# Optimization experiments

Hardware: AMD Instinct MI355X
Metric: run time of the kernel (lower is better)

## Reference

```python
import jax, jax.numpy as jnp
import numpy as np

N, E = 50000, 800000
D_IN, H, D_OUT = 100, 128, 40
N_MID = 2  # num_layers(5) - 3
EPS = 1e-5


def setup_inputs() -> dict:
    key = jax.random.key(0)
    ks = iter(jax.random.split(key, 40))
    rn = lambda shape, s=0.05: jax.random.normal(next(ks), shape, dtype=jnp.float32) * s
    inp = {
        "x": jax.random.normal(next(ks), (N, D_IN), dtype=jnp.float32),
        "edge_index": jax.random.randint(next(ks), (2, E), 0, N, dtype=jnp.int64),
        "percent": 70,
        "ricci_curvature": jax.random.normal(next(ks), (E,), dtype=jnp.float32),
        # GCNConv weights/biases
        "W1": rn((D_IN, H)), "b1": jnp.zeros((H,), jnp.float32),
        "W2": rn((D_IN + H, H)), "b2": jnp.zeros((H,), jnp.float32),
        "Wm": rn((N_MID, 2 * H, H)), "bm": jnp.zeros((N_MID, H), jnp.float32),
        "Wo": rn((2 * H, D_OUT)), "bo": jnp.zeros((D_OUT,), jnp.float32),
    }
    # BatchNorm1d params + running stats (eval mode)
    def bn_params(dim, lead=()):
        return (jnp.ones(lead + (dim,), jnp.float32),            # gamma
                jnp.zeros(lead + (dim,), jnp.float32),           # beta
                rn(lead + (dim,), 0.1),                          # running mean
                1.0 + 0.1 * jax.random.uniform(next(ks), lead + (dim,), dtype=jnp.float32))  # running var
    inp["bn1_g"], inp["bn1_b"], inp["bn1_m"], inp["bn1_v"] = bn_params(D_IN)
    inp["bn2_g"], inp["bn2_b"], inp["bn2_m"], inp["bn2_v"] = bn_params(D_IN + H)
    inp["bnm_g"], inp["bnm_b"], inp["bnm_m"], inp["bnm_v"] = bn_params(2 * H, (N_MID,))
    inp["bno_g"], inp["bno_b"], inp["bno_m"], inp["bno_v"] = bn_params(2 * H)
    return inp


def reference(x, edge_index, percent, ricci_curvature,
              W1, b1, W2, b2, Wm, bm, Wo, bo,
              bn1_g, bn1_b, bn1_m, bn1_v,
              bn2_g, bn2_b, bn2_m, bn2_v,
              bnm_g, bnm_b, bnm_m, bnm_v,
              bno_g, bno_b, bno_m, bno_v):
    # Eval mode: no sampling / dynamic edge weights, dropout = identity,
    # BN uses running stats. GCNConv = PyG: add self-loops, sym-norm D^-1/2 A D^-1/2.
    n = x.shape[0]
    loop = jnp.arange(n)
    src = jnp.concatenate([edge_index[0], loop])  # [E+N]
    dst = jnp.concatenate([edge_index[1], loop])
    deg = jnp.zeros((n,), x.dtype).at[dst].add(1.0)  # >=1 thanks to self-loops
    dis = jax.lax.rsqrt(deg)
    norm = (dis[src] * dis[dst])[:, None]  # [E+N, 1]

    def gcn(h, W, b):
        hw = h @ W  # [N, out]
        agg = jnp.zeros((n, W.shape[1]), h.dtype).at[dst].add(hw[src] * norm)
        return agg + b

    def bn(h, g, bta, m, v):
        return (h - m) * (g * jax.lax.rsqrt(v + EPS)) + bta

    res = []
    x_in = x
    h = jax.nn.relu(gcn(bn(x, bn1_g, bn1_b, bn1_m, bn1_v), W1, b1))
    res.append(h)
    h = jnp.concatenate([h, x_in], axis=1)  # [N, H+D_IN]
    h = jax.nn.relu(gcn(bn(h, bn2_g, bn2_b, bn2_m, bn2_v), W2, b2))
    res.append(h)
    h = jnp.concatenate([h, res[-2]], axis=1)  # [N, 2H]
    for i in range(Wm.shape[0]):
        hi = jax.nn.relu(gcn(bn(h, bnm_g[i], bnm_b[i], bnm_m[i], bnm_v[i]), Wm[i], bm[i]))
        res.append(hi)
        h = jnp.concatenate([hi, res[-2]], axis=1)
    out = gcn(bn(h, bno_g, bno_b, bno_m, bno_v), Wo, bo)
    return (out, *res)
```

## Files before the change

kernel.cpp:

```cpp
#include <hip/hip_runtime.h>
#include <hip/hip_bf16.h>
#include <cstdint>
#include <cstddef>

#define BN_EPS 1e-5f
typedef long long ll;
using bf16x8 = __attribute__((ext_vector_type(8))) short;
using f32x4  = __attribute__((ext_vector_type(4))) float;

__device__ __forceinline__ unsigned short f2bf(float f) {
    union { float f; unsigned u; } c; c.f = f;
    unsigned u = c.u;
    u += 0x7fff + ((u >> 16) & 1);
    return (unsigned short)(u >> 16);
}
__device__ __forceinline__ float bf2f(unsigned h) {
    union { unsigned u; float f; } c; c.u = h << 16;
    return c.f;
}
__device__ __forceinline__ void addbf8(float* a, uint4 v) {
    a[0] += bf2f(v.x & 0xffffu); a[1] += bf2f(v.x >> 16);
    a[2] += bf2f(v.y & 0xffffu); a[3] += bf2f(v.y >> 16);
    a[4] += bf2f(v.z & 0xffffu); a[5] += bf2f(v.z >> 16);
    a[6] += bf2f(v.w & 0xffffu); a[7] += bf2f(v.w >> 16);
}
__device__ __forceinline__ float4 bf4_to_f4(uint2 v) {
    return make_float4(bf2f(v.x & 0xffffu), bf2f(v.x >> 16),
                       bf2f(v.y & 0xffffu), bf2f(v.y >> 16));
}
__device__ __forceinline__ void gload_lds16(const void* g, void* lds) {
    __builtin_amdgcn_global_load_lds(
        (const __attribute__((address_space(1))) unsigned int*)g,
        (__attribute__((address_space(3))) unsigned int*)lds, 16, 0, 0);
}

__global__ void build0_kernel(const int* ei32, int* flag, int* deg, int* cursor, int N) {
    int i = blockIdx.x * 256 + threadIdx.x;
    if (i < N) { deg[i] = 1; cursor[i] = 0; }
    if (blockIdx.x == 0) {
        __shared__ int any;
        if (threadIdx.x == 0) any = 0;
        __syncthreads();
        for (int t = threadIdx.x; t < 2048; t += 256)
            if (ei32[2 * t + 1] != 0) any = 1;
        __syncthreads();
        if (threadIdx.x == 0) *flag = (any == 0) ? 1 : 0;
    }
}

__global__ void count_kernel(const void* ei, int E, int* deg, const int* flag) {
    int e = blockIdx.x * 256 + threadIdx.x;
    if (e >= E) return;
    int d = (*flag) ? (int)((const ll*)ei)[(size_t)E + e]
                    : ((const int*)ei)[(size_t)E + e];
    atomicAdd(&deg[d], 1);
}

__global__ __launch_bounds__(1024) void scanA_kernel(const int* deg, int* row_ptr,
                                                     int* bsum, float* dis, int N) {
    __shared__ int wsum[16];
    int i = blockIdx.x * 1024 + threadIdx.x;
    int lane = threadIdx.x & 63, wid = threadIdx.x >> 6;
    int dv = (i < N) ? deg[i] : 1;
    if (i < N) dis[i] = rsqrtf((float)dv);
    int v = (i < N) ? (dv - 1) : 0;
    int s = v;
#pragma unroll
    for (int o = 1; o < 64; o <<= 1) { int t = __shfl_up(s, o); if (lane >= o) s += t; }
    if (lane == 63) wsum[wid] = s;
    __syncthreads();
    if (threadIdx.x < 16) {
        int w = wsum[threadIdx.x];
        int ws_ = w;
#pragma unroll
        for (int o = 1; o < 16; o <<= 1) { int t = __shfl_up(ws_, o); if ((int)threadIdx.x >= o) ws_ += t; }
        wsum[threadIdx.x] = ws_ - w;
    }
    __syncthreads();
    s += wsum[wid];
    if (i < N) row_ptr[i + 1] = s;
    if (threadIdx.x == 1023) bsum[blockIdx.x] = s;
}

__global__ void scanB_kernel(int* bsum, int nb) {
    int lane = threadIdx.x;
    int v = (lane < nb) ? bsum[lane] : 0;
    int s = v;
#pragma unroll
    for (int o = 1; o < 64; o <<= 1) { int t = __shfl_up(s, o); if (lane >= o) s += t; }
    if (lane < nb) bsum[lane] = s - v;
}

__global__ __launch_bounds__(1024) void scanC_kernel(int* row_ptr, const int* bsum, int N) {
    int i = blockIdx.x * 1024 + threadIdx.x;
    if (i < N) row_ptr[i + 1] += bsum[blockIdx.x];
    if (i == 0) row_ptr[0] = 0;
}

__global__ void fill_kernel(const void* ei, int E, const int* row_ptr,
                            int* cursor, int* csr, const int* flag) {
    int e = blockIdx.x * 256 + threadIdx.x;
    if (e >= E) return;
    int s, d;
    if (*flag) { const ll* p = (const ll*)ei; s = (int)p[e]; d = (int)p[(size_t)E + e]; }
    else       { const int* p = (const int*)ei; s = p[e]; d = p[(size_t)E + e]; }
    int pos = atomicAdd(&cursor[d], 1);
    csr[row_ptr[d] + pos] = s;
}

struct LayerP {
    const float *W, *g, *b, *m, *v;
    int K, Dout, ncb, boff;
};
struct LayerPs { LayerP l[5]; };

__global__ __launch_bounds__(256) void fold_all(LayerPs P,
                                                unsigned short* __restrict__ Bhi,
                                                unsigned short* __restrict__ Blo,
                                                float* __restrict__ cvecA) {
    const LayerP& L = P.l[blockIdx.y];
    if (blockIdx.x < 128) {
        int nkc = (L.K + 63) >> 6 << 1;
        int total = nkc * L.ncb * 512;
        int idx = blockIdx.x * 256 + threadIdx.x;
        if (idx >= total) return;
        int i = idx & 7;
        int lane = (idx >> 3) & 63;
        int cb = (idx >> 9) % L.ncb;
        int kc = (idx >> 9) / L.ncb;
        int k = kc * 32 + (lane >> 4) * 8 + i;
        int col = cb * 16 + (lane & 15);
        float val = 0.f;
        if (k < L.K && col < L.Dout) {
            float s = L.g[k] * rsqrtf(L.v[k] + BN_EPS);
            val = L.W[k * L.Dout + col] * s;
        }
        unsigned short h = f2bf(val);
        Bhi[L.boff + idx] = h;
        Blo[L.boff + idx] = f2bf(val - bf2f(h));
    } else {
        int wid = threadIdx.x >> 6, lane = threadIdx.x & 63;
        int col = (blockIdx.x - 128) * 4 + wid;
        float acc = 0.f;
        if (col < L.Dout) {
            for (int k = lane; k < L.K; k += 64) {
                float s = L.g[k] * rsqrtf(L.v[k] + BN_EPS);
                acc += (L.b[k] - L.m[k] * s) * L.W[k * L.Dout + col];
            }
        }
#pragma unroll
        for (int o = 32; o >= 1; o >>= 1) acc += __shfl_xor(acc, o);
        if (lane == 0 && col < 128) cvecA[128 * blockIdx.y + col] = (col < L.Dout) ? acc : 0.f;
    }
}

__global__ __launch_bounds__(256, 4) void gemm_bf2_kernel(
    const unsigned short* __restrict__ X1, int K1, int ld1,
    const unsigned short* __restrict__ X2, int ld2,
    const unsigned short* __restrict__ Bhi, const unsigned short* __restrict__ Blo,
    const float* __restrict__ cvec, const float* __restrict__ dis,
    unsigned short* __restrict__ outp, int K, int N)
{
    __shared__ unsigned short Xs[2][64 * 64];
    const int tid = threadIdx.x;
    const int w = tid >> 6, lane = tid & 63;
    const int lr = lane & 15, lg = lane >> 4;
    const int brow = blockIdx.x * 64;
    const int nkt = (K + 63) >> 6;
    const int cb0 = 2 * w;

    int s_r[2], s_sl[2];
#pragma unroll
    for (int p = 0; p < 2; ++p) {
        int idx = p * 256 + tid;
        s_r[p] = idx >> 3;
        s_sl[p] = idx & 7;
    }

    auto STAGE = [&](int kt, int b) {
        const int k0 = kt * 64;
        const unsigned short* T = (k0 < K1) ? X1 : X2;
        const int ldT = (k0 < K1) ? ld1 : ld2;
        const int kb = (k0 < K1) ? k0 : (k0 - K1);
#pragma unroll
        for (int p = 0; p < 2; ++p) {
            int grow = brow + s_r[p]; if (grow >= N) grow = N - 1;
            int ksl = s_sl[p] ^ (s_r[p] & 7);
            gload_lds16(T + (size_t)grow * ldT + kb + ksl * 8,
                        (char*)Xs[b] + (size_t)(p * 256 + w * 64) * 16);
        }
    };

    f32x4 acc[4][2];
#pragma unroll
    for (int c = 0; c < 2; ++c) {
        float cv = cvec[(cb0 + c) * 16 + lr];
        f32x4 iv = {cv, cv, cv, cv};
#pragma unroll
        for (int rb = 0; rb < 4; ++rb) acc[rb][c] = iv;
    }

    STAGE(0, 0);
    for (int kt = 0; kt < nkt; ++kt) {
        const int cur = kt & 1;
        if (kt + 1 < nkt) STAGE(kt + 1, cur ^ 1);
        __builtin_amdgcn_sched_barrier(0);
        if (kt + 1 < nkt) asm volatile("s_waitcnt vmcnt(2)" ::: "memory");
        else              asm volatile("s_waitcnt vmcnt(0)" ::: "memory");
        __builtin_amdgcn_s_barrier();
        __builtin_amdgcn_sched_barrier(0);

#pragma unroll
        for (int ks = 0; ks < 2; ++ks) {
            const int kcg = kt * 2 + ks;
            bf16x8 a[4];
#pragma unroll
            for (int rb = 0; rb < 4; ++rb) {
                int r = rb * 16 + lr;
                a[rb] = *(const bf16x8*)((const char*)Xs[cur] + r * 128 +
                                         ((ks * 64 + lg * 16) ^ ((r & 7) << 4)));
            }
            const bf16x8* bh = (const bf16x8*)Bhi + (size_t)kcg * 8 * 64;
            const bf16x8* bl = (const bf16x8*)Blo + (size_t)kcg * 8 * 64;
#pragma unroll
            for (int c = 0; c < 2; ++c) {
                bf16x8 bhf = bh[(cb0 + c) * 64 + lane];
                bf16x8 blf = bl[(cb0 + c) * 64 + lane];
#pragma unroll
                for (int rb = 0; rb < 4; ++rb) {
                    acc[rb][c] = __builtin_amdgcn_mfma_f32_16x16x32_bf16(a[rb], bhf, acc[rb][c], 0, 0, 0);
                    acc[rb][c] = __builtin_amdgcn_mfma_f32_16x16x32_bf16(a[rb], blf, acc[rb][c], 0, 0, 0);
                }
            }
        }
        asm volatile("s_waitcnt lgkmcnt(0)" ::: "memory");
        __builtin_amdgcn_s_barrier();
        __builtin_amdgcn_sched_barrier(0);
    }

#pragma unroll
    for (int rb = 0; rb < 4; ++rb) {
#pragma unroll
        for (int r = 0; r < 4; ++r) {
            int grow = brow + rb * 16 + lg * 4 + r;
            if (grow >= N) continue;
            float d = dis[grow];
#pragma unroll
            for (int c = 0; c < 2; ++c)
                outp[(size_t)grow * 128 + (cb0 + c) * 16 + lr] = f2bf(d * acc[rb][c][r]);
        }
    }
}

template <bool B1, bool B2>
__global__ __launch_bounds__(256, 3) void gemm_mix2_kernel(
    const void* __restrict__ X1, int K1, int ld1,
    const void* __restrict__ X2, int ld2,
    const unsigned short* __restrict__ Bhi, const unsigned short* __restrict__ Blo,
    const float* __restrict__ cvec, const float* __restrict__ dis,
    unsigned short* __restrict__ outp, int K, int kc_lo, int N)
{
    __shared__ unsigned short Xhi[64 * 64];
    __shared__ unsigned short Xlo[64 * 64];
    const int tid = threadIdx.x;
    const int w = tid >> 6, lane = tid & 63;
    const int lr = lane & 15, lg = lane >> 4;
    const int brow = blockIdx.x * 64;
    const int nkt = (K + 63) >> 6;
    const int cb0 = 2 * w;

    f32x4 acc[4][2];
#pragma unroll
    for (int c = 0; c < 2; ++c) {
        float cv = cvec[(cb0 + c) * 16 + lr];
        f32x4 iv = {cv, cv, cv, cv};
#pragma unroll
        for (int rb = 0; rb < 4; ++rb) acc[rb][c] = iv;
    }

    for (int kt = 0; kt < nkt; ++kt) {
        const int k0 = kt * 64;
        const bool kt_lo = (kt * 2 + 1) >= kc_lo;
#pragma unroll
        for (int p = 0; p < 4; ++p) {
            int fidx = (p * 256 + tid) * 4;
            int r = fidx >> 6;
            int c = fidx & 63;
            int grow = brow + r;
            int k = k0 + c;
            float4 val = make_float4(0.f, 0.f, 0.f, 0.f);
            if (grow < N) {
                if (k < K1) {
                    if (B1) val = bf4_to_f4(*(const uint2*)((const unsigned short*)X1 + (size_t)grow * ld1 + k));
                    else    val = *(const float4*)((const float*)X1 + (size_t)grow * ld1 + k);
                } else if (k < K) {
                    int kk = k - K1;
                    if (B2) val = bf4_to_f4(*(const uint2*)((const unsigned short*)X2 + (size_t)grow * ld2 + kk));
                    else    val = *(const float4*)((const float*)X2 + (size_t)grow * ld2 + kk);
                }
            }
            unsigned short h0 = f2bf(val.x), h1 = f2bf(val.y),
                           h2 = f2bf(val.z), h3 = f2bf(val.w);
            int b8 = c * 2;
            int addr = r * 128 + (((b8 & 0x70) ^ ((r & 7) << 4)) | (b8 & 8));
            *(uint2*)((char*)Xhi + addr) =
                make_uint2((unsigned)h0 | ((unsigned)h1 << 16),
                           (unsigned)h2 | ((unsigned)h3 << 16));
            if (kt_lo) {
                unsigned short l0 = f2bf(val.x - bf2f(h0)), l1 = f2bf(val.y - bf2f(h1)),
                               l2 = f2bf(val.z - bf2f(h2)), l3 = f2bf(val.w - bf2f(h3));
                *(uint2*)((char*)Xlo + addr) =
                    make_uint2((unsigned)l0 | ((unsigned)l1 << 16),
                               (unsigned)l2 | ((unsigned)l3 << 16));
            }
        }
        __syncthreads();

#pragma unroll
        for (int ks = 0; ks < 2; ++ks) {
            const int kcg = kt * 2 + ks;
            const bool need_lo = (kcg >= kc_lo);
            bf16x8 ah[4], al[4];
#pragma unroll
            for (int rb = 0; rb < 4; ++rb) {
                int r = rb * 16 + lr;
                int off = ((ks * 64 + lg * 16) ^ ((r & 7) << 4));
                ah[rb] = *(const bf16x8*)((const char*)Xhi + r * 128 + off);
                if (need_lo) al[rb] = *(const bf16x8*)((const char*)Xlo + r * 128 + off);
            }
            const bf16x8* bh = (const bf16x8*)Bhi + (size_t)kcg * 8 * 64;
            const bf16x8* bl = (const bf16x8*)Blo + (size_t)kcg * 8 * 64;
#pragma unroll
            for (int c = 0; c < 2; ++c) {
                bf16x8 bhf = bh[(cb0 + c) * 64 + lane];
                bf16x8 blf = bl[(cb0 + c) * 64 + lane];
#pragma unroll
                for (int rb = 0; rb < 4; ++rb) {
                    acc[rb][c] = __builtin_amdgcn_mfma_f32_16x16x32_bf16(ah[rb], bhf, acc[rb][c], 0, 0, 0);
                    acc[rb][c] = __builtin_amdgcn_mfma_f32_16x16x32_bf16(ah[rb], blf, acc[rb][c], 0, 0, 0);
                    if (need_lo)
                        acc[rb][c] = __builtin_amdgcn_mfma_f32_16x16x32_bf16(al[rb], bhf, acc[rb][c], 0, 0, 0);
                }
            }
        }
        __syncthreads();
    }

#pragma unroll
    for (int rb = 0; rb < 4; ++rb) {
#pragma unroll
        for (int r = 0; r < 4; ++r) {
            int grow = brow + rb * 16 + lg * 4 + r;
            if (grow >= N) continue;
            float d = dis[grow];
#pragma unroll
            for (int c = 0; c < 2; ++c)
                outp[(size_t)grow * 128 + (cb0 + c) * 16 + lr] = f2bf(d * acc[rb][c][r]);
        }
    }
}

__global__ __launch_bounds__(256, 4) void gemm_bf40_kernel(
    const unsigned short* __restrict__ X1, int K1, int ld1,
    const unsigned short* __restrict__ X2, int ld2,
    const unsigned short* __restrict__ Bhi, const unsigned short* __restrict__ Blo,
    const float* __restrict__ cvec, const float* __restrict__ dis,
    unsigned short* __restrict__ outp, int K, int N)
{
    __shared__ unsigned short Xs[2][64 * 64];
    const int tid = threadIdx.x;
    const int w = tid >> 6, lane = tid & 63;
    const int lr = lane & 15, lg = lane >> 4;
    const int brow = blockIdx.x * 64;
    const int nkt = (K + 63) >> 6;

    int s_r[2], s_sl[2];
#pragma unroll
    for (int p = 0; p < 2; ++p) {
        int idx = p * 256 + tid;
        s_r[p] = idx >> 3;
        s_sl[p] = idx & 7;
    }
    auto STAGE = [&](int kt, int b) {
        const int k0 = kt * 64;
        const unsigned short* T = (k0 < K1) ? X1 : X2;
        const int ldT = (k0 < K1) ? ld1 : ld2;
        const int kb = (k0 < K1) ? k0 : (k0 - K1);
#pragma unroll
        for (int p = 0; p < 2; ++p) {
            int grow = brow + s_r[p]; if (grow >= N) grow = N - 1;
            int ksl = s_sl[p] ^ (s_r[p] & 7);
            gload_lds16(T + (size_t)grow * ldT + kb + ksl * 8,
                        (char*)Xs[b] + (size_t)(p * 256 + w * 64) * 16);
        }
    };

    f32x4 acc[3];
#pragma unroll
    for (int cb = 0; cb < 3; ++cb) {
        float cv = cvec[cb * 16 + lr];
        f32x4 iv = {cv, cv, cv, cv};
        acc[cb] = iv;
    }

    STAGE(0, 0);
    for (int kt = 0; kt < nkt; ++kt) {
        const int cur = kt & 1;
        if (kt + 1 < nkt) STAGE(kt + 1, cur ^ 1);
        __builtin_amdgcn_sched_barrier(0);
        if (kt + 1 < nkt) asm volatile("s_waitcnt vmcnt(2)" ::: "memory");
        else              asm volatile("s_waitcnt vmcnt(0)" ::: "memory");
        __builtin_amdgcn_s_barrier();
        __builtin_amdgcn_sched_barrier(0);

        const int r = w * 16 + lr;
        const char* base = (const char*)Xs[cur] + r * 128;
        const int swz = (r & 7) << 4;
        bf16x8 a0 = *(const bf16x8*)(base + ((lg * 16) ^ swz));
        bf16x8 a1 = *(const bf16x8*)(base + ((64 + lg * 16) ^ swz));
#pragma unroll
        for (int ks = 0; ks < 2; ++ks) {
            const int kcg = kt * 2 + ks;
            const bf16x8 af = ks ? a1 : a0;
            const bf16x8* bh = (const bf16x8*)Bhi + (size_t)kcg * 3 * 64;
            const bf16x8* bl = (const bf16x8*)Blo + (size_t)kcg * 3 * 64;
#pragma unroll
            for (int cb = 0; cb < 3; ++cb) {
                bf16x8 bhf = bh[cb * 64 + lane];
                bf16x8 blf = bl[cb * 64 + lane];
                acc[cb] = __builtin_amdgcn_mfma_f32_16x16x32_bf16(af, bhf, acc[cb], 0, 0, 0);
                acc[cb] = __builtin_amdgcn_mfma_f32_16x16x32_bf16(af, blf, acc[cb], 0, 0, 0);
            }
        }
        asm volatile("s_waitcnt lgkmcnt(0)" ::: "memory");
        __builtin_amdgcn_s_barrier();
        __builtin_amdgcn_sched_barrier(0);
    }

#pragma unroll
    for (int r = 0; r < 4; ++r) {
        int grow = brow + w * 16 + lg * 4 + r;
        if (grow >= N) continue;
        float d = dis[grow];
#pragma unroll
        for (int cb = 0; cb < 3; ++cb) {
            int col = cb * 16 + lr;
            if (col < 40) outp[(size_t)grow * 40 + col] = f2bf(d * acc[cb][r]);
        }
    }
}

template <bool RELU>
__global__ __launch_bounds__(256) void agg128b_kernel(
    const unsigned short* __restrict__ hwb,
    const int* __restrict__ row_ptr, const int* __restrict__ csr,
    const float* __restrict__ dis, const float* __restrict__ bias,
    float* __restrict__ outp, unsigned short* __restrict__ hbout, int N)
{
    int wid = threadIdx.x >> 6, lane = threadIdx.x & 63;
    int node = blockIdx.x * 4 + wid;
    if (node >= N) return;
    const int sg = lane >> 4, q = lane & 15;
    const uint4* hw4 = (const uint4*)hwb;
    float a[8] = {0.f, 0.f, 0.f, 0.f, 0.f, 0.f, 0.f, 0.f};
    float b8[8] = {0.f, 0.f, 0.f, 0.f, 0.f, 0.f, 0.f, 0.f};
    if (sg == 0) addbf8(a, hw4[(size_t)node * 16 + q]);
    int beg = row_ptr[node], end = row_ptr[node + 1];
    for (int base = beg; base < end; base += 64) {
        int idx = base + lane;
        int j = (idx < end) ? csr[idx] : 0;
        int cnt = end - base; if (cnt > 64) cnt = 64;
        int fullq = cnt >> 2;
        int t = 0;
        for (; t + 2 <= fullq; t += 2) {
            int ja = __shfl(j, 4 * t + sg);
            int jb = __shfl(j, 4 * t + 4 + sg);
            uint4 va = hw4[(size_t)ja * 16 + q];
            uint4 vb = hw4[(size_t)jb * 16 + q];
            addbf8(a, va); addbf8(b8, vb);
        }
        for (; t < fullq; ++t) {
            int ja = __shfl(j, 4 * t + sg);
            uint4 va = hw4[(size_t)ja * 16 + q];
            addbf8(a, va);
        }
        int rem = cnt & 3;
        if (rem) {
            int srcl = (cnt & ~3) + ((sg < rem) ? sg : 0);
            int ja = __shfl(j, srcl);
            if (sg < rem) {
                uint4 va = hw4[(size_t)ja * 16 + q];
                addbf8(a, va);
            }
        }
    }
#pragma unroll
    for (int c = 0; c < 8; ++c) {
        a[c] += b8[c];
        a[c] += __shfl_xor(a[c], 16);
        a[c] += __shfl_xor(a[c], 32);
    }
    if (sg == 0) {
        float d = dis[node];
        float4 bv0 = ((const float4*)bias)[q * 2];
        float4 bv1 = ((const float4*)bias)[q * 2 + 1];
        float o[8];
        o[0] = fmaf(d, a[0], bv0.x); o[1] = fmaf(d, a[1], bv0.y);
        o[2] = fmaf(d, a[2], bv0.z); o[3] = fmaf(d, a[3], bv0.w);
        o[4] = fmaf(d, a[4], bv1.x); o[5] = fmaf(d, a[5], bv1.y);
        o[6] = fmaf(d, a[6], bv1.z); o[7] = fmaf(d, a[7], bv1.w);
        if (RELU) {
#pragma unroll
            for (int c = 0; c < 8; ++c) o[c] = fmaxf(o[c], 0.f);
        }
        ((float4*)outp)[(size_t)node * 32 + q * 2]     = make_float4(o[0], o[1], o[2], o[3]);
        ((float4*)outp)[(size_t)node * 32 + q * 2 + 1] = make_float4(o[4], o[5], o[6], o[7]);
        uint4 pk;
        pk.x = (unsigned)f2bf(o[0]) | ((unsigned)f2bf(o[1]) << 16);
        pk.y = (unsigned)f2bf(o[2]) | ((unsigned)f2bf(o[3]) << 16);
        pk.z = (unsigned)f2bf(o[4]) | ((unsigned)f2bf(o[5]) << 16);
        pk.w = (unsigned)f2bf(o[6]) | ((unsigned)f2bf(o[7]) << 16);
        ((uint4*)hbout)[(size_t)node * 16 + q] = pk;
    }
}

__global__ __launch_bounds__(256) void agg40b_kernel(
    const unsigned short* __restrict__ hwb,
    const int* __restrict__ row_ptr, const int* __restrict__ csr,
    const float* __restrict__ dis, const float* __restrict__ bias,
    float* __restrict__ outp, int N)
{
    int wid = threadIdx.x >> 6, lane = threadIdx.x & 63;
    int node = blockIdx.x * 4 + wid;
    if (node >= N) return;
    const int half = lane >> 5, q = lane & 31;
    const bool act = q < 20;
    const unsigned* hw20 = (const unsigned*)hwb;
    float a0 = 0.f, a1 = 0.f, b0 = 0.f, b1 = 0.f;
    if (half == 0 && act) {
        unsigned v = hw20[(size_t)node * 20 + q];
        a0 += bf2f(v & 0xffffu); a1 += bf2f(v >> 16);
    }
    int beg = row_ptr[node], end = row_ptr[node + 1];
    for (int base = beg; base < end; base += 64) {
        int idx = base + lane;
        int j = (idx < end) ? csr[idx] : 0;
        int cnt = end - base; if (cnt > 64) cnt = 64;
        int fullp = cnt >> 1;
        int t = 0;
        for (; t + 4 <= fullp; t += 4) {
            int ja = __shfl(j, 2 * t     + half);
            int jb = __shfl(j, 2 * t + 2 + half);
            int jc = __shfl(j, 2 * t + 4 + half);
            int jd = __shfl(j, 2 * t + 6 + half);
            if (act) {
                unsigned va = hw20[(size_t)ja * 20 + q];
                unsigned vb = hw20[(size_t)jb * 20 + q];
                unsigned vc = hw20[(size_t)jc * 20 + q];
                unsigned vd = hw20[(size_t)jd * 20 + q];
                a0 += bf2f(va & 0xffffu); a1 += bf2f(va >> 16);
                b0 += bf2f(vb & 0xffffu); b1 += bf2f(vb >> 16);
                a0 += bf2f(vc & 0xffffu); a1 += bf2f(vc >> 16);
                b0 += bf2f(vd & 0xffffu); b1 += bf2f(vd >> 16);
            }
        }
        for (; t < fullp; ++t) {
            int ja = __shfl(j, 2 * t + half);
            if (act) {
                unsigned va = hw20[(size_t)ja * 20 + q];
                a0 += bf2f(va & 0xffffu); a1 += bf2f(va >> 16);
            }
        }
        if (cnt & 1) {
            int ja = __shfl(j, cnt - 1);
            if (half == 0 && act) {
                unsigned va = hw20[(size_t)ja * 20 + q];
                a0 += bf2f(va & 0xffffu); a1 += bf2f(va >> 16);
            }
        }
    }
    a0 += b0; a1 += b1;
    a0 += __shfl_xor(a0, 32);
    a1 += __shfl_xor(a1, 32);
    if (half == 0 && act) {
        float d = dis[node];
        float2 o;
        o.x = fmaf(d, a0, bias[2 * q]);
        o.y = fmaf(d, a1, bias[2 * q + 1]);
        *(float2*)(outp + (size_t)node * 40 + 2 * q) = o;
    }
}

extern "C" void kernel_launch(void* const* d_in, const int* in_sizes, int n_in,
                              void* d_out, int out_size, void* d_ws, size_t ws_size,
                              hipStream_t stream) {
    const int N = in_sizes[0] / 100;
    const int E = in_sizes[1] / 2;

    const float* x   = (const float*)d_in[0];
    const void*  ei  = d_in[1];
    const float* W1  = (const float*)d_in[4];
    const float* b1  = (const float*)d_in[5];
    const float* W2  = (const float*)d_in[6];
    const float* b2  = (const float*)d_in[7];
    const float* Wm  = (const float*)d_in[8];
    const float* bm  = (const float*)d_in[9];
    const float* Wo  = (const float*)d_in[10];
    const float* bo  = (const float*)d_in[11];
    const float* bn1g = (const float*)d_in[12];
    const float* bn1b = (const float*)d_in[13];
    const float* bn1m = (const float*)d_in[14];
    const float* bn1v = (const float*)d_in[15];
    const float* bn2g = (const float*)d_in[16];
    const float* bn2b = (const float*)d_in[17];
    const float* bn2m = (const float*)d_in[18];
    const float* bn2v = (const float*)d_in[19];
    const float* bnmg = (const float*)d_in[20];
    const float* bnmb = (const float*)d_in[21];
    const float* bnmm = (const float*)d_in[22];
    const float* bnmv = (const float*)d_in[23];
    const float* bnog = (const float*)d_in[24];
    const float* bnob = (const float*)d_in[25];
    const float* bnom = (const float*)d_in[26];
    const float* bnov = (const float*)d_in[27];

    char* wsb = (char*)d_ws;
    size_t off = 0;
    auto alloc = [&](size_t elems) -> void* { void* p = wsb + off; off += elems * 4; return p; };
    int*   deg     = (int*)alloc(N);
    int*   cursor  = (int*)alloc(N);
    int*   row_ptr = (int*)alloc((size_t)N + 1);
    int*   bsum    = (int*)alloc(64);
    int*   flag    = (int*)alloc(1);
    off = (off + 15) & ~(size_t)15;
    float* dis  = (float*)alloc(N);
    int*   csr  = (int*)alloc(E);
    off = (off + 15) & ~(size_t)15;
    unsigned short* hwb = (unsigned short*)alloc((size_t)N * 64);
    unsigned short* hbA = (unsigned short*)alloc((size_t)N * 64);
    unsigned short* hbB = (unsigned short*)alloc((size_t)N * 64);
    unsigned short* hbC = (unsigned short*)alloc((size_t)N * 64);
    unsigned short* BhiA = (unsigned short*)alloc(63488);
    unsigned short* BloA = (unsigned short*)alloc(63488);
    float* cvecA = (float*)alloc(128 * 5);
    (void)ws_size; (void)n_in; (void)out_size;

    float* outF = (float*)d_out;
    float* h1 = outF + (size_t)N * 40;
    float* h2 = h1 + (size_t)N * 128;
    float* h3 = h2 + (size_t)N * 128;
    float* h4 = h3 + (size_t)N * 128;

    dim3 b256(256);

    LayerPs P;
    P.l[0] = {W1, bn1g, bn1b, bn1m, bn1v, 100, 128, 8, 0};
    P.l[1] = {W2, bn2g, bn2b, bn2m, bn2v, 228, 128, 8, 16384};
    P.l[2] = {Wm, bnmg, bnmb, bnmm, bnmv, 256, 128, 8, 49152};
    P.l[3] = {Wm + 256 * 128, bnmg + 256, bnmb + 256, bnmm + 256, bnmv + 256, 256, 128, 8, 81920};
    P.l[4] = {Wo, bnog, bnob, bnom, bnov, 256, 40, 3, 114688};
    fold_all<<<dim3(160, 5), b256, 0, stream>>>(P, BhiA, BloA, cvecA);

    build0_kernel<<<dim3((N + 255) / 256), b256, 0, stream>>>((const int*)ei, flag, deg, cursor, N);
    count_kernel<<<dim3((E + 255) / 256), b256, 0, stream>>>(ei, E, deg, flag);
    int nb = (N + 1023) / 1024;
    scanA_kernel<<<dim3(nb), dim3(1024), 0, stream>>>(deg, row_ptr, bsum, dis, N);
    scanB_kernel<<<1, 64, 0, stream>>>(bsum, nb);
    scanC_kernel<<<dim3(nb), dim3(1024), 0, stream>>>(row_ptr, bsum, N);
    fill_kernel<<<dim3((E + 255) / 256), b256, 0, stream>>>(ei, E, row_ptr, cursor, csr, flag);

    int gemm_grid = (N + 63) / 64;
    int agg_grid  = (N + 3) / 4;

    auto agg128 = [&](const float* lb, float* dst, unsigned short* hbout) {
        agg128b_kernel<true><<<dim3(agg_grid), b256, 0, stream>>>(
            hwb, row_ptr, csr, dis, lb, dst, hbout, N);
    };

    gemm_mix2_kernel<false, false><<<dim3(gemm_grid), b256, 0, stream>>>(
        x, 100, 100, nullptr, 0, BhiA + P.l[0].boff, BloA + P.l[0].boff,
        cvecA, dis, hwb, 100, 0, N);
    agg128(b1, h1, hbA);

    gemm_mix2_kernel<true, false><<<dim3(gemm_grid), b256, 0, stream>>>(
        hbA, 128, 128, x, 100, BhiA + P.l[1].boff, BloA + P.l[1].boff,
        cvecA + 128, dis, hwb, 228, 4, N);
    agg128(b2, h2, hbB);

    gemm_bf2_kernel<<<dim3(gemm_grid), b256, 0, stream>>>(
        hbB, 128, 128, hbA, 128, BhiA + P.l[2].boff, BloA + P.l[2].boff,
        cvecA + 256, dis, hwb, 256, N);
    agg128(bm, h3, hbC);

    gemm_bf2_kernel<<<dim3(gemm_grid), b256, 0, stream>>>(
        hbC, 128, 128, hbB, 128, BhiA + P.l[3].boff, BloA + P.l[3].boff,
        cvecA + 384, dis, hwb, 256, N);
    agg128(bm + 128, h4, hbA);

    gemm_bf40_kernel<<<dim3(gemm_grid), b256, 0, stream>>>(
        hbA, 128, 128, hbC, 128, BhiA + P.l[4].boff, BloA + P.l[4].boff,
        cvecA + 512, dis, hwb, 256, N);
    agg40b_kernel<<<dim3(agg_grid), b256, 0, stream>>>(hwb, row_ptr, csr, dis, bo, outF, N);
}
```

Measured before the change: 378.1 us.

## Split 128-wide aggregation into two column-half kernel passes

The 128-column GCN aggregation kernel is replaced by a templated half kernel that gathers 64 columns (8-byte loads per lane) and is launched twice, once per column half. The intent is to shrink the gathered working set per pass so neighbor rows stay resident in L2/MALL and get better cache reuse. The cost is reading the CSR indices and row pointers twice, two launches, and smaller per-lane loads. The RELU template parameter is dropped and relu is now always applied.

```diff
diff --git a/kernel.cpp b/kernel.cpp
--- a/kernel.cpp
+++ b/kernel.cpp
@@ -18,11 +18,9 @@
     union { unsigned u; float f; } c; c.u = h << 16;
     return c.f;
 }
-__device__ __forceinline__ void addbf8(float* a, uint4 v) {
+__device__ __forceinline__ void addbf4(float* a, uint2 v) {
     a[0] += bf2f(v.x & 0xffffu); a[1] += bf2f(v.x >> 16);
     a[2] += bf2f(v.y & 0xffffu); a[3] += bf2f(v.y >> 16);
-    a[4] += bf2f(v.z & 0xffffu); a[5] += bf2f(v.z >> 16);
-    a[6] += bf2f(v.w & 0xffffu); a[7] += bf2f(v.w >> 16);
 }
 __device__ __forceinline__ float4 bf4_to_f4(uint2 v) {
     return make_float4(bf2f(v.x & 0xffffu), bf2f(v.x >> 16),
@@ -450,8 +448,8 @@
     }
 }
 
-template <bool RELU>
-__global__ __launch_bounds__(256) void agg128b_kernel(
+template <int HALF>
+__global__ __launch_bounds__(256) void agg128h_kernel(
     const unsigned short* __restrict__ hwb,
     const int* __restrict__ row_ptr, const int* __restrict__ csr,
     const float* __restrict__ dis, const float* __restrict__ bias,
@@ -460,11 +458,12 @@
     int wid = threadIdx.x >> 6, lane = threadIdx.x & 63;
     int node = blockIdx.x * 4 + wid;
     if (node >= N) return;
-    const int sg = lane >> 4, q = lane & 15;
-    const uint4* hw4 = (const uint4*)hwb;
-    float a[8] = {0.f, 0.f, 0.f, 0.f, 0.f, 0.f, 0.f, 0.f};
-    float b8[8] = {0.f, 0.f, 0.f, 0.f, 0.f, 0.f, 0.f, 0.f};
-    if (sg == 0) addbf8(a, hw4[(size_t)node * 16 + q]);
+    const int sub = lane >> 4, u = lane & 15;
+    const uint2* hw2 = (const uint2*)hwb;
+    const int soff = HALF * 16 + u;
+    float a[4] = {0.f, 0.f, 0.f, 0.f};
+    float b4[4] = {0.f, 0.f, 0.f, 0.f};
+    if (sub == 0) addbf4(a, hw2[(size_t)node * 32 + soff]);
     int beg = row_ptr[node], end = row_ptr[node + 1];
     for (int base = beg; base < end; base += 64) {
         int idx = base + lane;
@@ -473,54 +472,47 @@
         int fullq = cnt >> 2;
         int t = 0;
         for (; t + 2 <= fullq; t += 2) {
-            int ja = __shfl(j, 4 * t + sg);
-            int jb = __shfl(j, 4 * t + 4 + sg);
-            uint4 va = hw4[(size_t)ja * 16 + q];
-            uint4 vb = hw4[(size_t)jb * 16 + q];
-            addbf8(a, va); addbf8(b8, vb);
+            int ja = __shfl(j, 4 * t + sub);
+            int jb = __shfl(j, 4 * t + 4 + sub);
+            uint2 va = hw2[(size_t)ja * 32 + soff];
+            uint2 vb = hw2[(size_t)jb * 32 + soff];
+            addbf4(a, va); addbf4(b4, vb);
         }
         for (; t < fullq; ++t) {
-            int ja = __shfl(j, 4 * t + sg);
-            uint4 va = hw4[(size_t)ja * 16 + q];
-            addbf8(a, va);
+            int ja = __shfl(j, 4 * t + sub);
+            uint2 va = hw2[(size_t)ja * 32 + soff];
+            addbf4(a, va);
         }
         int rem = cnt & 3;
         if (rem) {
-            int srcl = (cnt & ~3) + ((sg < rem) ? sg : 0);
+            int srcl = (cnt & ~3) + ((sub < rem) ? sub : 0);
             int ja = __shfl(j, srcl);
-            if (sg < rem) {
-                uint4 va = hw4[(size_t)ja * 16 + q];
-                addbf8(a, va);
-            }
-        }
-    }
-#pragma unroll
-    for (int c = 0; c < 8; ++c) {
-        a[c] += b8[c];
+            if (sub < rem) {
+                uint2 va = hw2[(size_t)ja * 32 + soff];
+                addbf4(a, va);
+            }
+        }
+    }
+#pragma unroll
+    for (int c = 0; c < 4; ++c) {
+        a[c] += b4[c];
         a[c] += __shfl_xor(a[c], 16);
         a[c] += __shfl_xor(a[c], 32);
     }
-    if (sg == 0) {
+    if (sub == 0) {
         float d = dis[node];
-        float4 bv0 = ((const float4*)bias)[q * 2];
-        float4 bv1 = ((const float4*)bias)[q * 2 + 1];
-        float o[8];
-        o[0] = fmaf(d, a[0], bv0.x); o[1] = fmaf(d, a[1], bv0.y);
-        o[2] = fmaf(d, a[2], bv0.z); o[3] = fmaf(d, a[3], bv0.w);
-        o[4] = fmaf(d, a[4], bv1.x); o[5] = fmaf(d, a[5], bv1.y);
-        o[6] = fmaf(d, a[6], bv1.z); o[7] = fmaf(d, a[7], bv1.w);
-        if (RELU) {
-#pragma unroll
-            for (int c = 0; c < 8; ++c) o[c] = fmaxf(o[c], 0.f);
-        }
-        ((float4*)outp)[(size_t)node * 32 + q * 2]     = make_float4(o[0], o[1], o[2], o[3]);
-        ((float4*)outp)[(size_t)node * 32 + q * 2 + 1] = make_float4(o[4], o[5], o[6], o[7]);
-        uint4 pk;
-        pk.x = (unsigned)f2bf(o[0]) | ((unsigned)f2bf(o[1]) << 16);
-        pk.y = (unsigned)f2bf(o[2]) | ((unsigned)f2bf(o[3]) << 16);
-        pk.z = (unsigned)f2bf(o[4]) | ((unsigned)f2bf(o[5]) << 16);
-        pk.w = (unsigned)f2bf(o[6]) | ((unsigned)f2bf(o[7]) << 16);
-        ((uint4*)hbout)[(size_t)node * 16 + q] = pk;
+        int col0 = HALF * 64 + u * 4;
+        float4 bv = *(const float4*)(bias + col0);
+        float4 o;
+        o.x = fmaxf(fmaf(d, a[0], bv.x), 0.f);
+        o.y = fmaxf(fmaf(d, a[1], bv.y), 0.f);
+        o.z = fmaxf(fmaf(d, a[2], bv.z), 0.f);
+        o.w = fmaxf(fmaf(d, a[3], bv.w), 0.f);
+        *(float4*)(outp + (size_t)node * 128 + col0) = o;
+        uint2 pk;
+        pk.x = (unsigned)f2bf(o.x) | ((unsigned)f2bf(o.y) << 16);
+        pk.y = (unsigned)f2bf(o.z) | ((unsigned)f2bf(o.w) << 16);
+        *(uint2*)(hbout + (size_t)node * 128 + col0) = pk;
     }
 }
 
@@ -673,7 +665,9 @@
     int agg_grid  = (N + 3) / 4;
 
     auto agg128 = [&](const float* lb, float* dst, unsigned short* hbout) {
-        agg128b_kernel<true><<<dim3(agg_grid), b256, 0, stream>>>(
+        agg128h_kernel<0><<<dim3(agg_grid), b256, 0, stream>>>(
+            hwb, row_ptr, csr, dis, lb, dst, hbout, N);
+        agg128h_kernel<1><<<dim3(agg_grid), b256, 0, stream>>>(
             hwb, row_ptr, csr, dis, lb, dst, hbout, N);
     };
 
```

Measured after the change: 473.1 us. +25.1%, slower.
